# Optimization experiments

Hardware: AMD Instinct MI355X
Metric: run time of the kernel (lower is better)

## Reference

```python
import jax, jax.numpy as jnp
import numpy as np

B, DIN, DOUT, NW = 32768, 768, 768, 48
NH = NW // 3  # num_haar == num_mexican == num_morlet == 16 for NW=48
OMEGA0 = 5.0
LN_EPS = 1e-5


def setup_inputs() -> dict:
    key = jax.random.key(0)
    ks = jax.random.split(key, 6)
    x = jax.random.normal(ks[0], (B, DIN), dtype=jnp.float32)
    # kaiming-normal-ish fan_in init for linear layers, zero bias
    W = jax.random.normal(ks[1], (DOUT, DIN), dtype=jnp.float32) / np.sqrt(DIN)
    b = jnp.zeros((DOUT,), jnp.float32)
    Wp = jax.random.normal(ks[2], (NW, DIN), dtype=jnp.float32) / np.sqrt(DIN)
    bp = jnp.zeros((NW,), jnp.float32)
    Wc = jax.random.normal(ks[3], (DOUT, NW), dtype=jnp.float32) / np.sqrt(NW)
    bc = jnp.zeros((DOUT,), jnp.float32)
    # mixed-type init: per-family logspace scales / linspace translations
    scales = jnp.asarray(np.concatenate([
        np.logspace(-0.5, 0.5, NH),
        np.logspace(-0.3, 0.7, NH),
        np.logspace(-0.3, 0.7, NW - 2 * NH)]), jnp.float32)
    translations = jnp.asarray(np.concatenate([
        np.linspace(-1.5, 1.5, NH),
        np.linspace(-1.5, 1.5, NH),
        np.linspace(-1.5, 1.5, NW - 2 * NH)]), jnp.float32)
    gamma = jnp.ones((DOUT,), jnp.float32)
    beta = jnp.zeros((DOUT,), jnp.float32)
    return {"x": x, "W": W, "b": b, "Wp": Wp, "bp": bp, "Wc": Wc,
            "bc": bc, "scales": scales, "translations": translations,
            "gamma": gamma, "beta": beta}


def _wavelet_basis(s):
    # s: [B, NW] already scaled/translated; columns split by family
    dt = s.dtype
    sh = s[:, :NH]
    haar = (((sh >= 0) & (sh < 0.5)).astype(dt)
            - ((sh >= 0.5) & (sh < 1.0)).astype(dt))
    sm = s[:, NH:2 * NH]
    mexican = (1.0 - sm * sm) * jnp.exp(-0.5 * sm * sm)
    so = s[:, 2 * NH:]
    morlet = jnp.cos(OMEGA0 * so) * jnp.exp(-0.5 * so * so)
    return jnp.concatenate([haar, mexican, morlet], axis=1)


def reference(x, W, b, Wp, bp, Wc, bc, scales, translations, gamma, beta):
    direct = x @ W.T + b                              # [B, DOUT]
    wi = x @ Wp.T + bp                                # [B, NW]
    s = (wi - translations) / scales                  # [B, NW]
    wav = jax.nn.gelu(_wavelet_basis(s), approximate=False)
    wpath = wav @ Wc.T + bc                           # [B, DOUT]
    h = direct + wpath
    mu = jnp.mean(h, axis=-1, keepdims=True)
    var = jnp.mean((h - mu) ** 2, axis=-1, keepdims=True)
    return (h - mu) * jax.lax.rsqrt(var + LN_EPS) * gamma + beta
```

## Files before the change

### kernel.cpp

```cpp
#include <hip/hip_runtime.h>
#include <math.h>


#define B_SZ  32768
#define DIN   768
#define DOUT  768
#define NWAV  48

#define WF_OFF   0
#define WPH_OFF  589824
#define WPL_OFF  638976
#define WCF_OFF  688128

typedef short bf16x8 __attribute__((ext_vector_type(8)));
typedef float f32x16 __attribute__((ext_vector_type(16)));

__device__ __forceinline__ float bf2f(short u) {
    union { unsigned int i; float f; } v;
    v.i = ((unsigned int)(unsigned short)u) << 16;
    return v.f;
}
__device__ __forceinline__ short f2bf(float f) {
    union { float f; unsigned int i; } v; v.f = f;
    unsigned int r = v.i + 0x7FFFu + ((v.i >> 16) & 1u);
    return (short)(r >> 16);
}

__global__ __launch_bounds__(256) void pack_kernel(
    const float* __restrict__ W, const float* __restrict__ Wp,
    const float* __restrict__ Wc, short* __restrict__ ws)
{
    const int gw = (blockIdx.x * 256 + threadIdx.x) >> 6;
    const int L  = threadIdx.x & 63;
    const int lm = L & 31, half = L >> 5;

    if (gw < 1152) {
        const int cb = gw / 48, kb = gw % 48;
        const int row = cb * 32 + lm;
        const int k = kb * 16 + half * 8;
        bf16x8 o;
#pragma unroll
        for (int j = 0; j < 8; j++) o[j] = f2bf(W[(size_t)row * DIN + k + j]);
        *reinterpret_cast<bf16x8*>(&ws[WF_OFF + (size_t)gw * 512 + L * 8]) = o;
    } else if (gw < 1248) {
        const int t = gw - 1152;
        const int ct = t / 48, kb = t % 48;
        const int j = ct * 32 + lm;
        const int k = kb * 16 + half * 8;
        bf16x8 h, l;
#pragma unroll
        for (int jj = 0; jj < 8; jj++) {
            float v = (j < NWAV) ? Wp[(size_t)j * DIN + k + jj] : 0.f;
            const short hh = f2bf(v);
            h[jj] = hh;
            l[jj] = f2bf(v - bf2f(hh));
        }
        *reinterpret_cast<bf16x8*>(&ws[WPH_OFF + (size_t)t * 512 + L * 8]) = h;
        *reinterpret_cast<bf16x8*>(&ws[WPL_OFF + (size_t)t * 512 + L * 8]) = l;
    } else if (gw < 1320) {
        const int t = gw - 1248;
        const int cb = t / 3, kb = t % 3;
        const int row = cb * 32 + lm;
        const int k = kb * 16 + half * 8;
        bf16x8 o;
#pragma unroll
        for (int jj = 0; jj < 8; jj++) o[jj] = f2bf(Wc[(size_t)row * NWAV + k + jj]);
        *reinterpret_cast<bf16x8*>(&ws[WCF_OFF + (size_t)t * 512 + L * 8]) = o;
    }
}

__global__ __launch_bounds__(512, 2) void fused_kernel(
    const float* __restrict__ x, const short* __restrict__ ws,
    const float* __restrict__ Wp,
    const float* __restrict__ bp, const float* __restrict__ sc,
    const float* __restrict__ tr,
    const float* __restrict__ bb, const float* __restrict__ bc,
    const float* __restrict__ gm, const float* __restrict__ bt,
    float* __restrict__ out)
{
    __shared__ __align__(16) short xh[2][64 * 72];
    __shared__ __align__(16) short xl[2][64 * 72];
    __shared__ float redS[64 * 8], redQ[64 * 8];
    __shared__ float muA[64], rsA[64];

    const short* WF  = ws + WF_OFF;
    const short* WPH = ws + WPH_OFF;
    const short* WPL = ws + WPL_OFF;
    const short* WCF = ws + WCF_OFF;

    const int tid = threadIdx.x;
    const int r0  = blockIdx.x * 64;
    const int wv  = tid >> 6, L = tid & 63;
    const int lm  = L & 31, half = L >> 5;

    f32x16 acc[2][3];
#pragma unroll
    for (int rt = 0; rt < 2; rt++)
#pragma unroll
        for (int ct = 0; ct < 3; ct++)
#pragma unroll
            for (int g = 0; g < 16; g++) acc[rt][ct][g] = 0.f;
    f32x16 wacc;
#pragma unroll
    for (int g = 0; g < 16; g++) wacc[g] = 0.f;

    const int wrt = wv & 1, wct = wv >> 1;

    const int srow = tid >> 3;
    const int sk   = (tid & 7) * 8;

    {
        const float4* xp = reinterpret_cast<const float4*>(&x[(size_t)(r0 + srow) * DIN + sk]);
        const float4 v0 = xp[0], v1 = xp[1];
        const float f[8] = {v0.x, v0.y, v0.z, v0.w, v1.x, v1.y, v1.z, v1.w};
        bf16x8 hh, ll;
#pragma unroll
        for (int i = 0; i < 8; i++) {
            const short h = f2bf(f[i]);
            hh[i] = h;
            ll[i] = f2bf(f[i] - bf2f(h));
        }
        *reinterpret_cast<bf16x8*>(&xh[0][srow * 72 + sk]) = hh;
        *reinterpret_cast<bf16x8*>(&xl[0][srow * 72 + sk]) = ll;
    }
    __syncthreads();

    for (int k0i = 0; k0i < 12; ++k0i) {
        const int cur = k0i & 1;
        float4 v0, v1;
        if (k0i < 11) {
            const float4* xp = reinterpret_cast<const float4*>(
                &x[(size_t)(r0 + srow) * DIN + (k0i + 1) * 64 + sk]);
            v0 = xp[0]; v1 = xp[1];
        }
        const int kb0 = k0i * 4;

#pragma unroll
        for (int ks = 0; ks < 4; ++ks) {
            const bf16x8 a0 = *reinterpret_cast<bf16x8*>(&xh[cur][lm * 72 + ks * 16 + half * 8]);
            const bf16x8 a1 = *reinterpret_cast<bf16x8*>(&xh[cur][(32 + lm) * 72 + ks * 16 + half * 8]);
#pragma unroll
            for (int ct = 0; ct < 3; ++ct) {
                const bf16x8 b = *reinterpret_cast<const bf16x8*>(
                    &WF[((size_t)((wv * 3 + ct) * 48 + kb0 + ks)) * 512 + L * 8]);
                acc[0][ct] = __builtin_amdgcn_mfma_f32_32x32x16_bf16(a0, b, acc[0][ct], 0, 0, 0);
                acc[1][ct] = __builtin_amdgcn_mfma_f32_32x32x16_bf16(a1, b, acc[1][ct], 0, 0, 0);
            }
        }

        if (wv < 4) {
#pragma unroll
            for (int ks = 0; ks < 4; ++ks) {
                const bf16x8 ah = *reinterpret_cast<bf16x8*>(&xh[cur][(wrt * 32 + lm) * 72 + ks * 16 + half * 8]);
                const bf16x8 al = *reinterpret_cast<bf16x8*>(&xl[cur][(wrt * 32 + lm) * 72 + ks * 16 + half * 8]);
                const bf16x8 bh = *reinterpret_cast<const bf16x8*>(
                    &WPH[((size_t)(wct * 48 + kb0 + ks)) * 512 + L * 8]);
                const bf16x8 bl = *reinterpret_cast<const bf16x8*>(
                    &WPL[((size_t)(wct * 48 + kb0 + ks)) * 512 + L * 8]);
                wacc = __builtin_amdgcn_mfma_f32_32x32x16_bf16(ah, bl, wacc, 0, 0, 0);
                wacc = __builtin_amdgcn_mfma_f32_32x32x16_bf16(al, bh, wacc, 0, 0, 0);
                wacc = __builtin_amdgcn_mfma_f32_32x32x16_bf16(ah, bh, wacc, 0, 0, 0);
            }
        }

        if (k0i < 11) {
            const float f[8] = {v0.x, v0.y, v0.z, v0.w, v1.x, v1.y, v1.z, v1.w};
            bf16x8 hh, ll;
#pragma unroll
            for (int i = 0; i < 8; i++) {
                const short h = f2bf(f[i]);
                hh[i] = h;
                ll[i] = f2bf(f[i] - bf2f(h));
            }
            *reinterpret_cast<bf16x8*>(&xh[1 - cur][srow * 72 + sk]) = hh;
            *reinterpret_cast<bf16x8*>(&xl[1 - cur][srow * 72 + sk]) = ll;
        }
        __syncthreads();
    }

    short* wavL = &xh[0][0];
    if (wv < 4) {
        const int j = wct * 32 + lm;
        if (j < NWAV) {
            const float bpv = bp[j], scv = sc[j], trv = tr[j];
#pragma unroll
            for (int g = 0; g < 16; ++g) {
                const int rowl = wrt * 32 + (g & 3) + 8 * (g >> 2) + 4 * half;
                const float wi = wacc[g] + bpv;
                const float s = (wi - trv) / scv;
                float w;
                if (j < 16) {
                    const float dmin = fminf(fabsf(s), fminf(fabsf(s - 0.5f), fabsf(s - 1.0f)));
                    if (dmin < 2e-4f) {
                        const float* xr = &x[(size_t)(r0 + rowl) * DIN];
                        const float* wr = &Wp[(size_t)j * DIN];
                        double a0 = 0.0, a1 = 0.0, a2 = 0.0, a3 = 0.0;
                        for (int k = 0; k < DIN; k += 4) {
                            a0 = fma((double)xr[k + 0], (double)wr[k + 0], a0);
                            a1 = fma((double)xr[k + 1], (double)wr[k + 1], a1);
                            a2 = fma((double)xr[k + 2], (double)wr[k + 2], a2);
                            a3 = fma((double)xr[k + 3], (double)wr[k + 3], a3);
                        }
                        const double wid = ((a0 + a1) + (a2 + a3)) + (double)bpv;
                        const double sd = (wid - (double)trv) / (double)scv;
                        w = (sd >= 0.0 && sd < 0.5) ? 1.f : ((sd >= 0.5 && sd < 1.0) ? -1.f : 0.f);
                    } else {
                        w = (s >= 0.f && s < 0.5f) ? 1.f : ((s >= 0.5f && s < 1.f) ? -1.f : 0.f);
                    }
                } else if (j < 32) {
                    w = (1.f - s * s) * expf(-0.5f * s * s);
                } else {
                    w = cosf(5.f * s) * expf(-0.5f * s * s);
                }
                const float gel = 0.5f * w * (1.f + erff(w * 0.70710678118654752f));
                wavL[rowl * 72 + j] = f2bf(gel);
            }
        }
    }
    __syncthreads();

#pragma unroll
    for (int ks = 0; ks < 3; ++ks) {
        const bf16x8 a0 = *reinterpret_cast<bf16x8*>(&wavL[lm * 72 + ks * 16 + half * 8]);
        const bf16x8 a1 = *reinterpret_cast<bf16x8*>(&wavL[(32 + lm) * 72 + ks * 16 + half * 8]);
#pragma unroll
        for (int ct = 0; ct < 3; ++ct) {
            const bf16x8 b = *reinterpret_cast<const bf16x8*>(
                &WCF[((size_t)((wv * 3 + ct) * 3 + ks)) * 512 + L * 8]);
            acc[0][ct] = __builtin_amdgcn_mfma_f32_32x32x16_bf16(a0, b, acc[0][ct], 0, 0, 0);
            acc[1][ct] = __builtin_amdgcn_mfma_f32_32x32x16_bf16(a1, b, acc[1][ct], 0, 0, 0);
        }
    }

    float bias[3], gmv[3], btv[3];
#pragma unroll
    for (int ct = 0; ct < 3; ++ct) {
        const int col = wv * 96 + ct * 32 + lm;
        bias[ct] = bb[col] + bc[col];
        gmv[ct] = gm[col];
        btv[ct] = bt[col];
    }
#pragma unroll
    for (int rt = 0; rt < 2; ++rt) {
#pragma unroll
        for (int g = 0; g < 16; ++g) {
            const float v0 = acc[rt][0][g] + bias[0];
            const float v1 = acc[rt][1][g] + bias[1];
            const float v2 = acc[rt][2][g] + bias[2];
            acc[rt][0][g] = v0; acc[rt][1][g] = v1; acc[rt][2][g] = v2;
            float s1 = v0 + v1 + v2;
            float s2 = v0 * v0 + v1 * v1 + v2 * v2;
            s1 += __shfl_xor(s1, 1);  s2 += __shfl_xor(s2, 1);
            s1 += __shfl_xor(s1, 2);  s2 += __shfl_xor(s2, 2);
            s1 += __shfl_xor(s1, 4);  s2 += __shfl_xor(s2, 4);
            s1 += __shfl_xor(s1, 8);  s2 += __shfl_xor(s2, 8);
            s1 += __shfl_xor(s1, 16); s2 += __shfl_xor(s2, 16);
            if (lm == 0) {
                const int rowl = rt * 32 + (g & 3) + 8 * (g >> 2) + 4 * half;
                redS[rowl * 8 + wv] = s1;
                redQ[rowl * 8 + wv] = s2;
            }
        }
    }
    __syncthreads();
    if (tid < 64) {
        float S = 0.f, Q = 0.f;
#pragma unroll
        for (int i = 0; i < 8; i++) { S += redS[tid * 8 + i]; Q += redQ[tid * 8 + i]; }
        const float mu = S * (1.f / 768.f);
        const float var = Q * (1.f / 768.f) - mu * mu;
        muA[tid] = mu;
        rsA[tid] = rsqrtf(var + 1e-5f);
    }
    __syncthreads();

#pragma unroll
    for (int rt = 0; rt < 2; ++rt) {
#pragma unroll
        for (int g = 0; g < 16; ++g) {
            const int rowl = rt * 32 + (g & 3) + 8 * (g >> 2) + 4 * half;
            const float mu = muA[rowl], rs = rsA[rowl];
            float* orow = &out[(size_t)(r0 + rowl) * DOUT + wv * 96 + lm];
#pragma unroll
            for (int ct = 0; ct < 3; ++ct) {
                orow[ct * 32] = (acc[rt][ct][g] - mu) * rs * gmv[ct] + btv[ct];
            }
        }
    }
}

extern "C" void kernel_launch(void* const* d_in, const int* in_sizes, int n_in,
                              void* d_out, int out_size, void* d_ws, size_t ws_size,
                              hipStream_t stream)
{
    const float* x  = (const float*)d_in[0];
    const float* W  = (const float*)d_in[1];
    const float* b  = (const float*)d_in[2];
    const float* Wp = (const float*)d_in[3];
    const float* bp = (const float*)d_in[4];
    const float* Wc = (const float*)d_in[5];
    const float* bc = (const float*)d_in[6];
    const float* sc = (const float*)d_in[7];
    const float* tr = (const float*)d_in[8];
    const float* gm = (const float*)d_in[9];
    const float* bt = (const float*)d_in[10];
    float* out = (float*)d_out;
    short* ws  = (short*)d_ws;

    pack_kernel<<<dim3(330), dim3(256), 0, stream>>>(W, Wp, Wc, ws);
    fused_kernel<<<dim3(B_SZ / 64), dim3(512), 0, stream>>>(
        x, ws, Wp, bp, sc, tr, b, bc, gm, bt, out);
}
```

Before: 308.1 us.

## Defer near-boundary Haar rows to a separate fp64 fix-up kernel

Instead of recomputing the Haar projection in double precision inline inside the fused GEMM kernel when a value falls near a step boundary, the fused kernel now appends the row index to a global worklist via an atomic counter. A new fix_kernel then recomputes each listed row entirely in fp64/fp32 (direct GEMM row, wavelet path, layernorm) and overwrites the output. This removes divergent, serial double-precision loops from the hot kernel, at the cost of an extra launch, atomics, and a fixed worklist capacity that could silently drop rows if overflowed.

```diff
diff --git a/kernel.cpp b/kernel.cpp
--- a/kernel.cpp
+++ b/kernel.cpp
@@ -11,6 +11,8 @@
 #define WPH_OFF  589824
 #define WPL_OFF  638976
 #define WCF_OFF  688128
+#define WL_OFF   724992
+#define WL_CAP   8192
 
 typedef short bf16x8 __attribute__((ext_vector_type(8)));
 typedef float f32x16 __attribute__((ext_vector_type(16)));
@@ -30,6 +32,9 @@
     const float* __restrict__ W, const float* __restrict__ Wp,
     const float* __restrict__ Wc, short* __restrict__ ws)
 {
+    if (blockIdx.x == 0 && threadIdx.x == 0)
+        *reinterpret_cast<unsigned*>(ws + WL_OFF) = 0u;
+
     const int gw = (blockIdx.x * 256 + threadIdx.x) >> 6;
     const int L  = threadIdx.x & 63;
     const int lm = L & 31, half = L >> 5;
@@ -71,7 +76,7 @@
 
 __global__ __launch_bounds__(512, 2) void fused_kernel(
     const float* __restrict__ x, const short* __restrict__ ws,
-    const float* __restrict__ Wp,
+    unsigned* __restrict__ wl,
     const float* __restrict__ bp, const float* __restrict__ sc,
     const float* __restrict__ tr,
     const float* __restrict__ bb, const float* __restrict__ bc,
@@ -192,21 +197,10 @@
                 if (j < 16) {
                     const float dmin = fminf(fabsf(s), fminf(fabsf(s - 0.5f), fabsf(s - 1.0f)));
                     if (dmin < 2e-4f) {
-                        const float* xr = &x[(size_t)(r0 + rowl) * DIN];
-                        const float* wr = &Wp[(size_t)j * DIN];
-                        double a0 = 0.0, a1 = 0.0, a2 = 0.0, a3 = 0.0;
-                        for (int k = 0; k < DIN; k += 4) {
-                            a0 = fma((double)xr[k + 0], (double)wr[k + 0], a0);
-                            a1 = fma((double)xr[k + 1], (double)wr[k + 1], a1);
-                            a2 = fma((double)xr[k + 2], (double)wr[k + 2], a2);
-                            a3 = fma((double)xr[k + 3], (double)wr[k + 3], a3);
-                        }
-                        const double wid = ((a0 + a1) + (a2 + a3)) + (double)bpv;
-                        const double sd = (wid - (double)trv) / (double)scv;
-                        w = (sd >= 0.0 && sd < 0.5) ? 1.f : ((sd >= 0.5 && sd < 1.0) ? -1.f : 0.f);
-                    } else {
-                        w = (s >= 0.f && s < 0.5f) ? 1.f : ((s >= 0.5f && s < 1.f) ? -1.f : 0.f);
+                        const unsigned idx = atomicAdd(&wl[0], 1u);
+                        if (idx < WL_CAP - 1) wl[1 + idx] = (unsigned)(r0 + rowl);
                     }
+                    w = (s >= 0.f && s < 0.5f) ? 1.f : ((s >= 0.5f && s < 1.f) ? -1.f : 0.f);
                 } else if (j < 32) {
                     w = (1.f - s * s) * expf(-0.5f * s * s);
                 } else {
@@ -286,6 +280,107 @@
                 orow[ct * 32] = (acc[rt][ct][g] - mu) * rs * gmv[ct] + btv[ct];
             }
         }
+    }
+}
+
+__global__ __launch_bounds__(256) void fix_kernel(
+    const float* __restrict__ x, const float* __restrict__ W,
+    const float* __restrict__ bb, const float* __restrict__ Wp,
+    const float* __restrict__ bp, const float* __restrict__ Wc,
+    const float* __restrict__ bc, const float* __restrict__ sc,
+    const float* __restrict__ tr, const float* __restrict__ gm,
+    const float* __restrict__ bt, const unsigned* __restrict__ wl,
+    float* __restrict__ out)
+{
+    __shared__ float  xrow[DIN];
+    __shared__ double wpart[NWAV][4];
+    __shared__ float  wavS[NWAV];
+    __shared__ float  hrow[DOUT];
+    __shared__ float  redS2[4], redQ2[4];
+    __shared__ float  mu_s, rs_s;
+
+    unsigned cnt = wl[0];
+    if (cnt > WL_CAP - 1) cnt = WL_CAP - 1;
+    const int tid = threadIdx.x;
+
+    for (unsigned it = blockIdx.x; it < cnt; it += gridDim.x) {
+        const int row = (int)wl[1 + it];
+
+        for (int k = tid; k < DIN; k += 256) xrow[k] = x[(size_t)row * DIN + k];
+        __syncthreads();
+
+        if (tid < NWAV * 4) {
+            const int j = tid >> 2, q = tid & 3;
+            const float* wr = &Wp[(size_t)j * DIN + q * 192];
+            const float* xr = &xrow[q * 192];
+            double a0 = 0.0, a1 = 0.0, a2 = 0.0, a3 = 0.0;
+            for (int k = 0; k < 192; k += 4) {
+                a0 = fma((double)xr[k + 0], (double)wr[k + 0], a0);
+                a1 = fma((double)xr[k + 1], (double)wr[k + 1], a1);
+                a2 = fma((double)xr[k + 2], (double)wr[k + 2], a2);
+                a3 = fma((double)xr[k + 3], (double)wr[k + 3], a3);
+            }
+            wpart[j][q] = (a0 + a1) + (a2 + a3);
+        }
+        __syncthreads();
+        if (tid < NWAV) {
+            const int j = tid;
+            const double wid = ((wpart[j][0] + wpart[j][1]) +
+                                (wpart[j][2] + wpart[j][3])) + (double)bp[j];
+            const double sd = (wid - (double)tr[j]) / (double)sc[j];
+            double w;
+            if (j < 16) {
+                w = (sd >= 0.0 && sd < 0.5) ? 1.0 : ((sd >= 0.5 && sd < 1.0) ? -1.0 : 0.0);
+            } else if (j < 32) {
+                w = (1.0 - sd * sd) * exp(-0.5 * sd * sd);
+            } else {
+                w = cos(5.0 * sd) * exp(-0.5 * sd * sd);
+            }
+            const double gel = 0.5 * w * (1.0 + erf(w * 0.70710678118654752));
+            wavS[j] = (float)gel;
+        }
+        __syncthreads();
+
+        for (int c = tid; c < DOUT; c += 256) {
+            const float* wr = &W[(size_t)c * DIN];
+            double a0 = 0.0, a1 = 0.0, a2 = 0.0, a3 = 0.0;
+            for (int k = 0; k < DIN; k += 4) {
+                a0 = fma((double)xrow[k + 0], (double)wr[k + 0], a0);
+                a1 = fma((double)xrow[k + 1], (double)wr[k + 1], a1);
+                a2 = fma((double)xrow[k + 2], (double)wr[k + 2], a2);
+                a3 = fma((double)xrow[k + 3], (double)wr[k + 3], a3);
+            }
+            float wp_ = 0.f;
+            const float* wcr = &Wc[(size_t)c * NWAV];
+#pragma unroll
+            for (int j = 0; j < NWAV; j++) wp_ += wavS[j] * wcr[j];
+            hrow[c] = (float)((a0 + a1) + (a2 + a3)) + bb[c] + wp_ + bc[c];
+        }
+        __syncthreads();
+
+        float S = 0.f, Q = 0.f;
+        for (int c = tid; c < DOUT; c += 256) { const float v = hrow[c]; S += v; Q += v * v; }
+        S += __shfl_xor(S, 1);  Q += __shfl_xor(Q, 1);
+        S += __shfl_xor(S, 2);  Q += __shfl_xor(Q, 2);
+        S += __shfl_xor(S, 4);  Q += __shfl_xor(Q, 4);
+        S += __shfl_xor(S, 8);  Q += __shfl_xor(Q, 8);
+        S += __shfl_xor(S, 16); Q += __shfl_xor(Q, 16);
+        S += __shfl_xor(S, 32); Q += __shfl_xor(Q, 32);
+        if ((tid & 63) == 0) { redS2[tid >> 6] = S; redQ2[tid >> 6] = Q; }
+        __syncthreads();
+        if (tid == 0) {
+            float Ss = 0.f, Qs = 0.f;
+#pragma unroll
+            for (int i = 0; i < 4; i++) { Ss += redS2[i]; Qs += redQ2[i]; }
+            const float mu = Ss * (1.f / 768.f);
+            const float var = Qs * (1.f / 768.f) - mu * mu;
+            mu_s = mu;
+            rs_s = rsqrtf(var + 1e-5f);
+        }
+        __syncthreads();
+        for (int c = tid; c < DOUT; c += 256)
+            out[(size_t)row * DOUT + c] = (hrow[c] - mu_s) * rs_s * gm[c] + bt[c];
+        __syncthreads();
     }
 }
 
@@ -306,8 +401,11 @@
     const float* bt = (const float*)d_in[10];
     float* out = (float*)d_out;
     short* ws  = (short*)d_ws;
+    unsigned* wl = reinterpret_cast<unsigned*>(ws + WL_OFF);
 
     pack_kernel<<<dim3(330), dim3(256), 0, stream>>>(W, Wp, Wc, ws);
     fused_kernel<<<dim3(B_SZ / 64), dim3(512), 0, stream>>>(
-        x, ws, Wp, bp, sc, tr, b, bc, gm, bt, out);
-}
+        x, ws, wl, bp, sc, tr, b, bc, gm, bt, out);
+    fix_kernel<<<dim3(256), dim3(256), 0, stream>>>(
+        x, W, b, Wp, bp, Wc, bc, sc, tr, gm, bt, wl, out);
+}
```

After: 361.6 us. 1.17x slower.

## Prefetch weight fragments per K-step, reuse A fragments, and block-cooperative haar fallback

Applied to the files above, without the earlier changes.

Loads all weight B-fragments for a K-step into registers before the MFMA loop so their global latency overlaps, and reuses the already-loaded xh A-fragment for the wavelet-projection MFMAs instead of reloading it. Replaces the per-lane serial double-precision recompute for near-boundary haar values with flags in shared memory and a block-wide cooperative dot product with shuffle reduction. Also makes the wave index wave-uniform via readfirstlane. In exchange, register pressure rises from the prefetched fragments, and each flagged element adds two block barriers.

```diff
diff --git a/kernel.cpp b/kernel.cpp
--- a/kernel.cpp
+++ b/kernel.cpp
@@ -82,6 +82,8 @@
     __shared__ __align__(16) short xl[2][64 * 72];
     __shared__ float redS[64 * 8], redQ[64 * 8];
     __shared__ float muA[64], rsA[64];
+    __shared__ unsigned flags[64];
+    __shared__ double dred[8];
 
     const short* WF  = ws + WF_OFF;
     const short* WPH = ws + WPH_OFF;
@@ -90,8 +92,16 @@
 
     const int tid = threadIdx.x;
     const int r0  = blockIdx.x * 64;
-    const int wv  = tid >> 6, L = tid & 63;
+    const int L   = tid & 63;
+    const int wv  = __builtin_amdgcn_readfirstlane(tid >> 6);
     const int lm  = L & 31, half = L >> 5;
+    const int L8  = L * 8;
+    const bool wi = (wv < 4);
+    const int wv3 = wv * 3;
+    const int wrt = wv & 1, wct = wv >> 1;
+    const int wct48 = wct * 48;
+
+    if (tid < 64) flags[tid] = 0u;
 
     f32x16 acc[2][3];
 #pragma unroll
@@ -103,8 +113,6 @@
     f32x16 wacc;
 #pragma unroll
     for (int g = 0; g < 16; g++) wacc[g] = 0.f;
-
-    const int wrt = wv & 1, wct = wv >> 1;
 
     const int srow = tid >> 3;
     const int sk   = (tid & 7) * 8;
@@ -127,39 +135,51 @@
 
     for (int k0i = 0; k0i < 12; ++k0i) {
         const int cur = k0i & 1;
+        const int kb0 = k0i * 4;
+
         float4 v0, v1;
         if (k0i < 11) {
             const float4* xp = reinterpret_cast<const float4*>(
                 &x[(size_t)(r0 + srow) * DIN + (k0i + 1) * 64 + sk]);
             v0 = xp[0]; v1 = xp[1];
         }
-        const int kb0 = k0i * 4;
+
+        bf16x8 bfr[4][3];
+#pragma unroll
+        for (int ks = 0; ks < 4; ++ks)
+#pragma unroll
+            for (int ct = 0; ct < 3; ++ct)
+                bfr[ks][ct] = *reinterpret_cast<const bf16x8*>(
+                    &WF[((size_t)((wv3 + ct) * 48 + kb0 + ks)) * 512 + L8]);
+        bf16x8 bwh[4], bwl[4];
+        if (wi) {
+#pragma unroll
+            for (int ks = 0; ks < 4; ++ks) {
+                bwh[ks] = *reinterpret_cast<const bf16x8*>(
+                    &WPH[((size_t)(wct48 + kb0 + ks)) * 512 + L8]);
+                bwl[ks] = *reinterpret_cast<const bf16x8*>(
+                    &WPL[((size_t)(wct48 + kb0 + ks)) * 512 + L8]);
+            }
+        }
 
 #pragma unroll
         for (int ks = 0; ks < 4; ++ks) {
-            const bf16x8 a0 = *reinterpret_cast<bf16x8*>(&xh[cur][lm * 72 + ks * 16 + half * 8]);
-            const bf16x8 a1 = *reinterpret_cast<bf16x8*>(&xh[cur][(32 + lm) * 72 + ks * 16 + half * 8]);
+            const bf16x8 a0 = *reinterpret_cast<bf16x8*>(
+                &xh[cur][lm * 72 + ks * 16 + half * 8]);
+            const bf16x8 a1 = *reinterpret_cast<bf16x8*>(
+                &xh[cur][(32 + lm) * 72 + ks * 16 + half * 8]);
 #pragma unroll
             for (int ct = 0; ct < 3; ++ct) {
-                const bf16x8 b = *reinterpret_cast<const bf16x8*>(
-                    &WF[((size_t)((wv * 3 + ct) * 48 + kb0 + ks)) * 512 + L * 8]);
-                acc[0][ct] = __builtin_amdgcn_mfma_f32_32x32x16_bf16(a0, b, acc[0][ct], 0, 0, 0);
-                acc[1][ct] = __builtin_amdgcn_mfma_f32_32x32x16_bf16(a1, b, acc[1][ct], 0, 0, 0);
-            }
-        }
-
-        if (wv < 4) {
-#pragma unroll
-            for (int ks = 0; ks < 4; ++ks) {
-                const bf16x8 ah = *reinterpret_cast<bf16x8*>(&xh[cur][(wrt * 32 + lm) * 72 + ks * 16 + half * 8]);
-                const bf16x8 al = *reinterpret_cast<bf16x8*>(&xl[cur][(wrt * 32 + lm) * 72 + ks * 16 + half * 8]);
-                const bf16x8 bh = *reinterpret_cast<const bf16x8*>(
-                    &WPH[((size_t)(wct * 48 + kb0 + ks)) * 512 + L * 8]);
-                const bf16x8 bl = *reinterpret_cast<const bf16x8*>(
-                    &WPL[((size_t)(wct * 48 + kb0 + ks)) * 512 + L * 8]);
-                wacc = __builtin_amdgcn_mfma_f32_32x32x16_bf16(ah, bl, wacc, 0, 0, 0);
-                wacc = __builtin_amdgcn_mfma_f32_32x32x16_bf16(al, bh, wacc, 0, 0, 0);
-                wacc = __builtin_amdgcn_mfma_f32_32x32x16_bf16(ah, bh, wacc, 0, 0, 0);
+                acc[0][ct] = __builtin_amdgcn_mfma_f32_32x32x16_bf16(a0, bfr[ks][ct], acc[0][ct], 0, 0, 0);
+                acc[1][ct] = __builtin_amdgcn_mfma_f32_32x32x16_bf16(a1, bfr[ks][ct], acc[1][ct], 0, 0, 0);
+            }
+            if (wi) {
+                const bf16x8 ah = wrt ? a1 : a0;
+                const bf16x8 al = *reinterpret_cast<bf16x8*>(
+                    &xl[cur][(wrt * 32 + lm) * 72 + ks * 16 + half * 8]);
+                wacc = __builtin_amdgcn_mfma_f32_32x32x16_bf16(ah, bwl[ks], wacc, 0, 0, 0);
+                wacc = __builtin_amdgcn_mfma_f32_32x32x16_bf16(al, bwh[ks], wacc, 0, 0, 0);
+                wacc = __builtin_amdgcn_mfma_f32_32x32x16_bf16(ah, bwh[ks], wacc, 0, 0, 0);
             }
         }
 
@@ -179,34 +199,20 @@
     }
 
     short* wavL = &xh[0][0];
-    if (wv < 4) {
+    if (wi) {
         const int j = wct * 32 + lm;
         if (j < NWAV) {
             const float bpv = bp[j], scv = sc[j], trv = tr[j];
 #pragma unroll
             for (int g = 0; g < 16; ++g) {
                 const int rowl = wrt * 32 + (g & 3) + 8 * (g >> 2) + 4 * half;
-                const float wi = wacc[g] + bpv;
-                const float s = (wi - trv) / scv;
+                const float wiv = wacc[g] + bpv;
+                const float s = (wiv - trv) / scv;
                 float w;
                 if (j < 16) {
                     const float dmin = fminf(fabsf(s), fminf(fabsf(s - 0.5f), fabsf(s - 1.0f)));
-                    if (dmin < 2e-4f) {
-                        const float* xr = &x[(size_t)(r0 + rowl) * DIN];
-                        const float* wr = &Wp[(size_t)j * DIN];
-                        double a0 = 0.0, a1 = 0.0, a2 = 0.0, a3 = 0.0;
-                        for (int k = 0; k < DIN; k += 4) {
-                            a0 = fma((double)xr[k + 0], (double)wr[k + 0], a0);
-                            a1 = fma((double)xr[k + 1], (double)wr[k + 1], a1);
-                            a2 = fma((double)xr[k + 2], (double)wr[k + 2], a2);
-                            a3 = fma((double)xr[k + 3], (double)wr[k + 3], a3);
-                        }
-                        const double wid = ((a0 + a1) + (a2 + a3)) + (double)bpv;
-                        const double sd = (wid - (double)trv) / (double)scv;
-                        w = (sd >= 0.0 && sd < 0.5) ? 1.f : ((sd >= 0.5 && sd < 1.0) ? -1.f : 0.f);
-                    } else {
-                        w = (s >= 0.f && s < 0.5f) ? 1.f : ((s >= 0.5f && s < 1.f) ? -1.f : 0.f);
-                    }
+                    if (dmin < 2e-4f) atomicOr(&flags[rowl], 1u << j);
+                    w = (s >= 0.f && s < 0.5f) ? 1.f : ((s >= 0.5f && s < 1.f) ? -1.f : 0.f);
                 } else if (j < 32) {
                     w = (1.f - s * s) * expf(-0.5f * s * s);
                 } else {
@@ -219,6 +225,36 @@
     }
     __syncthreads();
 
+#pragma unroll 1
+    for (int fr = 0; fr < 64; ++fr) {
+        unsigned m = flags[fr];
+        while (m) {
+            const int j = __ffs(m) - 1;
+            m &= m - 1;
+            const float* xr = &x[(size_t)(r0 + fr) * DIN];
+            const float* wr = &Wp[(size_t)j * DIN];
+            double a = (double)xr[tid] * (double)wr[tid];
+            if (tid < DIN - 512)
+                a += (double)xr[tid + 512] * (double)wr[tid + 512];
+            a += __shfl_xor(a, 1);  a += __shfl_xor(a, 2);
+            a += __shfl_xor(a, 4);  a += __shfl_xor(a, 8);
+            a += __shfl_xor(a, 16); a += __shfl_xor(a, 32);
+            if (L == 0) dred[wv] = a;
+            __syncthreads();
+            if (tid == 0) {
+                double wid = (double)bp[j];
+#pragma unroll
+                for (int i = 0; i < 8; i++) wid += dred[i];
+                const double sd = (wid - (double)tr[j]) / (double)sc[j];
+                const double w = (sd >= 0.0 && sd < 0.5) ? 1.0
+                               : ((sd >= 0.5 && sd < 1.0) ? -1.0 : 0.0);
+                const double gel = 0.5 * w * (1.0 + erf(w * 0.70710678118654752));
+                wavL[fr * 72 + j] = f2bf((float)gel);
+            }
+            __syncthreads();
+        }
+    }
+
 #pragma unroll
     for (int ks = 0; ks < 3; ++ks) {
         const bf16x8 a0 = *reinterpret_cast<bf16x8*>(&wavL[lm * 72 + ks * 16 + half * 8]);
@@ -226,7 +262,7 @@
 #pragma unroll
         for (int ct = 0; ct < 3; ++ct) {
             const bf16x8 b = *reinterpret_cast<const bf16x8*>(
-                &WCF[((size_t)((wv * 3 + ct) * 3 + ks)) * 512 + L * 8]);
+                &WCF[((size_t)((wv3 + ct) * 3 + ks)) * 512 + L8]);
             acc[0][ct] = __builtin_amdgcn_mfma_f32_32x32x16_bf16(a0, b, acc[0][ct], 0, 0, 0);
             acc[1][ct] = __builtin_amdgcn_mfma_f32_32x32x16_bf16(a1, b, acc[1][ct], 0, 0, 0);
         }
```

After: 267.8 us. 1.15x faster.
